# Kernel tuning notes

Measured on AMD Instinct MI355X. Metric: run time of the kernel, lower is better.

## Reference

```python
import jax, jax.numpy as jnp
import numpy as np

N = 50000      # nodes
E = 800000     # edges (avg degree 16)
IN = 128       # in_channels
OUT = 64       # out_channels
HID = 2 * OUT  # 128, hidden width of conv1
EPS = 1e-5     # BatchNorm eps


def _edge_norm(edge_index):
    # PyG ChebConv with sym normalization, lambda_max=2: L_hat = -D^{-1/2} A D^{-1/2}
    src, dst = edge_index[0], edge_index[1]
    deg = jax.ops.segment_sum(jnp.ones((E,), jnp.float32), src, num_segments=N)
    dinv = jnp.where(deg > 0, jax.lax.rsqrt(jnp.maximum(deg, 1.0)), 0.0)
    return -dinv[src] * dinv[dst]


def _cheb(x, src, dst, norm, W0, W1, b):
    # K=2 Chebyshev conv: Tx0 = x, Tx1 = L_hat x (sparse propagate)
    tx1 = jax.ops.segment_sum(x[src] * norm[:, None], dst, num_segments=N)
    return x @ W0 + tx1 @ W1 + b


def setup_inputs() -> dict:
    key = jax.random.key(0)
    ks = jax.random.split(key, 14)
    g = lambda k, shp, fan: jax.random.normal(k, shp, jnp.float32) / np.sqrt(fan)
    return {
        "x": jax.random.normal(ks[0], (N, IN), jnp.float32),
        "edge_index": jax.random.randint(ks[1], (2, E), 0, N, dtype=jnp.int32),
        "W1_0": g(ks[2], (IN, HID), IN),
        "W1_1": g(ks[3], (IN, HID), IN),
        "b1": jnp.zeros((HID,), jnp.float32),
        "gamma": jnp.ones((HID,), jnp.float32),
        "beta": jnp.zeros((HID,), jnp.float32),
        "Wmu_0": g(ks[4], (HID, OUT), HID),
        "Wmu_1": g(ks[5], (HID, OUT), HID),
        "b_mu": jnp.zeros((OUT,), jnp.float32),
        "Wls_0": g(ks[6], (HID, OUT), HID),
        "Wls_1": g(ks[7], (HID, OUT), HID),
        "b_ls": jnp.zeros((OUT,), jnp.float32),
    }


def reference(x, edge_index, W1_0, W1_1, b1, gamma, beta,
              Wmu_0, Wmu_1, b_mu, Wls_0, Wls_1, b_ls):
    src, dst = edge_index[0], edge_index[1]
    norm = _edge_norm(edge_index)
    h = _cheb(x, src, dst, norm, W1_0, W1_1, b1)         # [N, HID]
    # BatchNorm1d (training mode: batch statistics over nodes)
    mean = jnp.mean(h, axis=0)
    var = jnp.var(h, axis=0)
    h = (h - mean) * jax.lax.rsqrt(var + EPS) * gamma + beta
    h = jax.nn.relu(h)
    mu = _cheb(h, src, dst, norm, Wmu_0, Wmu_1, b_mu)    # [N, OUT]
    logstd = _cheb(h, src, dst, norm, Wls_0, Wls_1, b_ls)
    return (mu, logstd)
```

## Files before the change

kernel.cpp:

```cpp
#include <hip/hip_runtime.h>
#include <cstddef>
#include <cstdint>

static constexpr int IN_C  = 128;
static constexpr float BN_EPS = 1e-5f;
static constexpr int OUT_C = 64;

static constexpr int CS_C = 32;
static constexpr int CS_R = 8;
static constexpr int CS_RANGE = 6250;

using bf16x8 = __attribute__((ext_vector_type(8))) short;
using f32x4  = __attribute__((ext_vector_type(4))) float;

__device__ __forceinline__ ushort f2bf(float f) {
    uint u = __float_as_uint(f);
    u += 0x7fffu + ((u >> 16) & 1u);
    return (ushort)(u >> 16);
}
__device__ __forceinline__ uint pack2(float a, float b) {
    return (uint)f2bf(a) | ((uint)f2bf(b) << 16);
}
__device__ __forceinline__ float bf_lo(uint v) { return __uint_as_float(v << 16); }
__device__ __forceinline__ float bf_hi(uint v) { return __uint_as_float(v & 0xffff0000u); }

__device__ __forceinline__ int swz8(int row, int g) { return (g ^ ((row >> 1) & 3)) * 8; }

__global__ __launch_bounds__(1024) void hist_k(
    const int* __restrict__ src, const int* __restrict__ dst,
    int* __restrict__ hsrc_part, int* __restrict__ hdst_part,
    int N, int E, int chunk, int range) {
    __shared__ int hs_[CS_RANGE];
    __shared__ int hd_[CS_RANGE];
    int c = blockIdx.x & (CS_C - 1);
    int r = blockIdx.x / CS_C;
    int base = r * range;
    int hi = min(base + range, N);
    int rsz = hi - base;
    for (int j = threadIdx.x; j < rsz; j += 1024) { hs_[j] = 0; hd_[j] = 0; }
    __syncthreads();
    int e0 = c * chunk, e1 = min(e0 + chunk, E);
    for (int i = e0 + threadIdx.x; i < e1; i += 1024) {
        int s = src[i];
        if (s >= base && s < hi) atomicAdd(&hs_[s - base], 1);
        int t = dst[i];
        if (t >= base && t < hi) atomicAdd(&hd_[t - base], 1);
    }
    __syncthreads();
    for (int j = threadIdx.x; j < rsz; j += 1024) {
        hsrc_part[(size_t)c * N + base + j] = hs_[j];
        hdst_part[(size_t)c * N + base + j] = hd_[j];
    }
}

__global__ __launch_bounds__(256) void count_k(
    const int* __restrict__ hsrc_part, const int* __restrict__ hdst_part,
    float* __restrict__ dinv, int* __restrict__ cnt_dst,
    int* __restrict__ bsum, float* __restrict__ stats, int N) {
    __shared__ int sw[4];
    int tid = threadIdx.x;
    if (blockIdx.x == 0) stats[tid] = 0.f;
    int v = blockIdx.x * 256 + tid;
    int b = 0;
    if (v < N) {
        int a = 0;
        for (int c = 0; c < CS_C; ++c) {
            a += hsrc_part[(size_t)c * N + v];
            b += hdst_part[(size_t)c * N + v];
        }
        dinv[v] = (a > 0) ? rsqrtf((float)a) : 0.f;
        cnt_dst[v] = b;
    }
    int t = b;
    #pragma unroll
    for (int off = 1; off < 64; off <<= 1) t += __shfl_xor(t, off, 64);
    if ((tid & 63) == 0) sw[tid >> 6] = t;
    __syncthreads();
    if (tid == 0) bsum[blockIdx.x] = sw[0] + sw[1] + sw[2] + sw[3];
}

__global__ __launch_bounds__(256) void bscan_k(int* __restrict__ bsum, int nb) {
    __shared__ int sm[256];
    int tid = threadIdx.x;
    int v = (tid < nb) ? bsum[tid] : 0;
    sm[tid] = v;
    __syncthreads();
    #pragma unroll
    for (int off = 1; off < 256; off <<= 1) {
        int t = (tid >= off) ? sm[tid - off] : 0;
        __syncthreads();
        sm[tid] += t;
        __syncthreads();
    }
    if (tid < nb) bsum[tid] = sm[tid] - v;
}

__global__ __launch_bounds__(256) void phase3_k(
    const int* __restrict__ cnt, const int* __restrict__ bsum,
    int* __restrict__ row_ptr, int* __restrict__ hdst_part, int n) {
    __shared__ int swv[4];
    int tid = threadIdx.x;
    int lane = tid & 63, wave = tid >> 6;
    int v = blockIdx.x * 256 + tid;
    int c = (v < n) ? cnt[v] : 0;
    int s = c;
    #pragma unroll
    for (int off = 1; off < 64; off <<= 1) {
        int t = __shfl_up(s, off, 64);
        if (lane >= off) s += t;
    }
    if (lane == 63) swv[wave] = s;
    __syncthreads();
    int wexcl = 0;
    for (int w = 0; w < wave; ++w) wexcl += swv[w];
    int st = bsum[blockIdx.x] + wexcl + (s - c);
    if (v < n) row_ptr[v + 1] = st + c;
    if (v == 0) row_ptr[0] = 0;
    int r = st;
    for (int ch = 0; ch < CS_C; ++ch) {
        size_t idx = (size_t)ch * n + v;
        if (v < n) {
            int t = hdst_part[idx];
            hdst_part[idx] = r;
            r += t;
        }
    }
}

__global__ __launch_bounds__(1024) void scatter_k(
    const int* __restrict__ src, const int* __restrict__ dst,
    const int* __restrict__ off, int* __restrict__ col,
    int N, int E, int chunk, int range) {
    __shared__ int cur[CS_RANGE];
    int c = blockIdx.x & (CS_C - 1);
    int r = blockIdx.x / CS_C;
    int base = r * range;
    int hi = min(base + range, N);
    int rsz = hi - base;
    for (int j = threadIdx.x; j < rsz; j += 1024)
        cur[j] = off[(size_t)c * N + base + j];
    __syncthreads();
    int e0 = c * chunk, e1 = min(e0 + chunk, E);
    for (int i = e0 + threadIdx.x; i < e1; i += 1024) {
        int t = dst[i];
        if (t >= base && t < hi) {
            int pos = atomicAdd(&cur[t - base], 1);
            col[pos] = src[i];
        }
    }
}

__global__ void convert_prep_k(const float* __restrict__ in, const float* __restrict__ dinv,
                               ushort* __restrict__ xb, ushort* __restrict__ xsb, int n64,
                               int nb_conv,
                               const float* __restrict__ W1_0, const float* __restrict__ W1_1,
                               const float* __restrict__ b1,
                               const float* __restrict__ Wmu_0, const float* __restrict__ Wmu_1,
                               const float* __restrict__ b_mu,
                               const float* __restrict__ Wls_0, const float* __restrict__ Wls_1,
                               const float* __restrict__ b_ls,
                               ushort* __restrict__ Wt1, ushort* __restrict__ Wt2,
                               float* __restrict__ bias1, float* __restrict__ bias2) {
    int bid = blockIdx.x;
    if (bid < nb_conv) {
        int i = bid * 256 + threadIdx.x;
        if (i >= n64) return;
        int row = i >> 6;
        float d = dinv[row];
        float2 v = ((const float2*)in)[i];
        ((uint*)xb)[i] = pack2(v.x, v.y);
        ((uint*)xsb)[i] = pack2(v.x * d, v.y * d);
    } else {
        int idx = (bid - nb_conv) * 256 + threadIdx.x;
        int which = idx >> 15;
        int c = (idx >> 8) & 127;
        int k = idx & 255;
        if (which == 0) {
            float v = (k < 128) ? W1_0[k * 128 + c] : W1_1[(k - 128) * 128 + c];
            Wt1[c * 256 + k] = f2bf(v);
            if (k == 0) bias1[c] = b1[c];
        } else {
            float v;
            if (c < 64) v = (k < 128) ? Wmu_0[k * 64 + c] : Wmu_1[(k - 128) * 64 + c];
            else        v = (k < 128) ? Wls_0[k * 64 + (c - 64)] : Wls_1[(k - 128) * 64 + (c - 64)];
            Wt2[c * 256 + k] = f2bf(v);
            if (k == 0) bias2[c] = (c < 64) ? b_mu[c] : b_ls[c - 64];
        }
    }
}

#define ACC8(V)                                         \
    acc[0] += bf_lo((V).x); acc[1] += bf_hi((V).x);     \
    acc[2] += bf_lo((V).y); acc[3] += bf_hi((V).y);     \
    acc[4] += bf_lo((V).z); acc[5] += bf_hi((V).z);     \
    acc[6] += bf_lo((V).w); acc[7] += bf_hi((V).w);

__global__ __launch_bounds__(256) void propagate4_k(
    const uint4* __restrict__ xs, uint4* __restrict__ out,
    const int* __restrict__ row_ptr, const int* __restrict__ col,
    const float* __restrict__ dinv, int n) {
    int wid = (blockIdx.x * 256 + threadIdx.x) >> 6;
    if (wid >= n) return;
    int lane = threadIdx.x & 63;
    int g = lane >> 4, li = lane & 15;
    int s = row_ptr[wid], e = row_ptr[wid + 1];
    float acc[8];
    #pragma unroll
    for (int k = 0; k < 8; ++k) acc[k] = 0.f;
    int i = s + g;
    for (; i + 12 < e; i += 16) {
        int c0 = col[i];
        int c1 = col[i + 4];
        int c2 = col[i + 8];
        int c3 = col[i + 12];
        uint4 v0 = xs[(size_t)c0 * 16 + li];
        uint4 v1 = xs[(size_t)c1 * 16 + li];
        uint4 v2 = xs[(size_t)c2 * 16 + li];
        uint4 v3 = xs[(size_t)c3 * 16 + li];
        ACC8(v0); ACC8(v1); ACC8(v2); ACC8(v3);
    }
    for (; i < e; i += 4) {
        int c0 = col[i];
        uint4 v0 = xs[(size_t)c0 * 16 + li];
        ACC8(v0);
    }
    #pragma unroll
    for (int k = 0; k < 8; ++k) {
        acc[k] += __shfl_xor(acc[k], 16, 64);
        acc[k] += __shfl_xor(acc[k], 32, 64);
    }
    if (g == 0) {
        float sc = -dinv[wid];
        uint4 o;
        o.x = pack2(acc[0] * sc, acc[1] * sc);
        o.y = pack2(acc[2] * sc, acc[3] * sc);
        o.z = pack2(acc[4] * sc, acc[5] * sc);
        o.w = pack2(acc[6] * sc, acc[7] * sc);
        out[(size_t)wid * 16 + li] = o;
    }
}

template <int MODE>
__global__ __launch_bounds__(256) void gemm_mfma_k(
    const ushort* __restrict__ A0, const ushort* __restrict__ A1,
    const ushort* __restrict__ Wt, const float* __restrict__ bias,
    ushort* __restrict__ Cb, float* __restrict__ Cmu, float* __restrict__ Cls,
    float* __restrict__ stats, int n) {
    __shared__ ushort sA[64][32];
    __shared__ ushort sW[128][32];
    __shared__ float smS[4][128];
    __shared__ float smQ[4][128];

    int tid = threadIdx.x;
    int block_row = blockIdx.x * 64;
    int wave = tid >> 6, lane = tid & 63;
    int col_base = lane & 15;
    int quad = lane >> 4;
    int m_local = wave * 16 + col_base;

    f32x4 acc[8];
    #pragma unroll
    for (int t = 0; t < 8; ++t) acc[t] = (f32x4){0.f, 0.f, 0.f, 0.f};

    for (int k0 = 0; k0 < 256; k0 += 32) {
        {
            int row = tid >> 2, g = tid & 3;
            int grow = block_row + row;
            int kc = k0 + g * 8;
            uint4 v = make_uint4(0, 0, 0, 0);
            if (grow < n) {
                const ushort* srcp = (kc < 128) ? (A0 + (size_t)grow * 128 + kc)
                                                : (A1 + (size_t)grow * 128 + (kc - 128));
                v = *(const uint4*)srcp;
            }
            *(uint4*)&sA[row][swz8(row, g)] = v;
        }
        #pragma unroll
        for (int i = tid; i < 512; i += 256) {
            int c = i >> 2, g = i & 3;
            *(uint4*)&sW[c][swz8(c, g)] = *(const uint4*)(Wt + (size_t)c * 256 + k0 + g * 8);
        }
        __syncthreads();
        bf16x8 af = *(const bf16x8*)&sA[m_local][swz8(m_local, quad)];
        #pragma unroll
        for (int t = 0; t < 8; ++t) {
            int wr = t * 16 + col_base;
            bf16x8 bfr = *(const bf16x8*)&sW[wr][swz8(wr, quad)];
            acc[t] = __builtin_amdgcn_mfma_f32_16x16x32_bf16(af, bfr, acc[t], 0, 0, 0);
        }
        __syncthreads();
    }

    int row_l = wave * 16 + quad * 4;
    #pragma unroll
    for (int t = 0; t < 8; ++t) {
        int col = t * 16 + col_base;
        float b = bias[col];
        float s = 0.f, q = 0.f;
        #pragma unroll
        for (int r = 0; r < 4; ++r) {
            int grow = block_row + row_l + r;
            if (grow < n) {
                float v = acc[t][r] + b;
                if (MODE == 0) {
                    Cb[(size_t)grow * 128 + col] = f2bf(v);
                    s += v; q += v * v;
                } else {
                    if (col < 64) Cmu[(size_t)grow * 64 + col] = v;
                    else          Cls[(size_t)grow * 64 + (col - 64)] = v;
                }
            }
        }
        if (MODE == 0) {
            s += __shfl_xor(s, 16, 64); s += __shfl_xor(s, 32, 64);
            q += __shfl_xor(q, 16, 64); q += __shfl_xor(q, 32, 64);
            if (quad == 0) { smS[wave][col] = s; smQ[wave][col] = q; }
        }
    }
    if (MODE == 0) {
        __syncthreads();
        if (tid < 128) {
            float s = smS[0][tid] + smS[1][tid] + smS[2][tid] + smS[3][tid];
            float q = smQ[0][tid] + smQ[1][tid] + smQ[2][tid] + smQ[3][tid];
            atomicAdd(&stats[tid], s);
            atomicAdd(&stats[128 + tid], q);
        }
    }
}

__global__ __launch_bounds__(256) void bn_apply_k(
    ushort* __restrict__ hb, ushort* __restrict__ hsb,
    const float* __restrict__ stats, const float* __restrict__ gamma,
    const float* __restrict__ beta, const float* __restrict__ dinv,
    float inv_n, int n64) {
    __shared__ float sp[256];
    int tid = threadIdx.x;
    if (tid < 128) {
        float mean = stats[tid] * inv_n;
        float var = stats[128 + tid] * inv_n - mean * mean;
        float sc = gamma[tid] * rsqrtf(var + BN_EPS);
        sp[tid] = sc;
        sp[128 + tid] = beta[tid] - mean * sc;
    }
    __syncthreads();
    int i = blockIdx.x * 256 + tid;
    if (i >= n64) return;
    int c2 = (i & 63) * 2;
    int row = i >> 6;
    uint v = ((uint*)hb)[i];
    float f0 = fmaxf(bf_lo(v) * sp[c2]     + sp[128 + c2],     0.f);
    float f1 = fmaxf(bf_hi(v) * sp[c2 + 1] + sp[128 + c2 + 1], 0.f);
    ((uint*)hb)[i] = pack2(f0, f1);
    float d = dinv[row];
    ((uint*)hsb)[i] = pack2(f0 * d, f1 * d);
}

extern "C" void kernel_launch(void* const* d_in, const int* in_sizes, int n_in,
                              void* d_out, int out_size, void* d_ws, size_t ws_size,
                              hipStream_t stream) {
    const float* x = (const float*)d_in[0];
    const int* edge_index = (const int*)d_in[1];
    const float* W1_0 = (const float*)d_in[2];
    const float* W1_1 = (const float*)d_in[3];
    const float* b1 = (const float*)d_in[4];
    const float* gamma = (const float*)d_in[5];
    const float* beta = (const float*)d_in[6];
    const float* Wmu_0 = (const float*)d_in[7];
    const float* Wmu_1 = (const float*)d_in[8];
    const float* b_mu = (const float*)d_in[9];
    const float* Wls_0 = (const float*)d_in[10];
    const float* Wls_1 = (const float*)d_in[11];
    const float* b_ls = (const float*)d_in[12];

    const int N = in_sizes[0] / IN_C;
    const int E = in_sizes[1] / 2;
    const int* src = edge_index;
    const int* dst = edge_index + E;

    char* w = (char*)d_ws;
    auto alloc = [&](size_t bytes) {
        char* p = w;
        w += (bytes + 15) & ~(size_t)15;
        return p;
    };
    float* stats = (float*)alloc(256 * 4);
    int* row_ptr = (int*)alloc((size_t)(N + 1) * 4);
    int* bsum    = (int*)alloc(256 * 4);
    float* dinv  = (float*)alloc((size_t)N * 4);
    int* cnt_dst = (int*)alloc((size_t)N * 4);
    int* col     = (int*)alloc((size_t)E * 4);
    int* hsrc_part = (int*)alloc((size_t)CS_C * N * 4);
    int* hdst_part = (int*)alloc((size_t)CS_C * N * 4);
    ushort* x_bf  = (ushort*)alloc((size_t)N * 128 * 2);
    ushort* xs_bf = (ushort*)alloc((size_t)N * 128 * 2);
    ushort* xp_bf = (ushort*)alloc((size_t)N * 128 * 2);
    ushort* h_bf  = (ushort*)alloc((size_t)N * 128 * 2);
    ushort* Wt1   = (ushort*)alloc(128 * 256 * 2);
    ushort* Wt2   = (ushort*)alloc(128 * 256 * 2);
    float* bias1  = (float*)alloc(128 * 4);
    float* bias2  = (float*)alloc(128 * 4);

    ushort* hs_bf = xs_bf;
    ushort* hp_bf = xp_bf;

    float* out_mu = (float*)d_out;
    float* out_ls = out_mu + (size_t)N * OUT_C;

    int chunk = (E + CS_C - 1) / CS_C;
    int range = (N + CS_R - 1) / CS_R;
    int NBLK = (N + 255) / 256;
    int nb_conv = (N * 64 + 255) / 256;

    hist_k<<<CS_R * CS_C, 1024, 0, stream>>>(src, dst, hsrc_part, hdst_part, N, E, chunk, range);
    count_k<<<NBLK, 256, 0, stream>>>(hsrc_part, hdst_part, dinv, cnt_dst, bsum, stats, N);
    bscan_k<<<1, 256, 0, stream>>>(bsum, NBLK);
    phase3_k<<<NBLK, 256, 0, stream>>>(cnt_dst, bsum, row_ptr, hdst_part, N);
    scatter_k<<<CS_R * CS_C, 1024, 0, stream>>>(src, dst, hdst_part, col, N, E, chunk, range);

    convert_prep_k<<<nb_conv + 256, 256, 0, stream>>>(
        x, dinv, x_bf, xs_bf, N * 64, nb_conv,
        W1_0, W1_1, b1, Wmu_0, Wmu_1, b_mu, Wls_0, Wls_1, b_ls,
        Wt1, Wt2, bias1, bias2);

    int pb = (N + 3) / 4;
    propagate4_k<<<pb, 256, 0, stream>>>((const uint4*)xs_bf, (uint4*)xp_bf,
                                         row_ptr, col, dinv, N);

    int gb = (N + 63) / 64;
    gemm_mfma_k<0><<<gb, 256, 0, stream>>>(x_bf, xp_bf, Wt1, bias1, h_bf,
                                           nullptr, nullptr, stats, N);

    bn_apply_k<<<(N * 64 + 255) / 256, 256, 0, stream>>>(h_bf, hs_bf, stats, gamma, beta,
                                                         dinv, 1.f / (float)N, N * 64);

    propagate4_k<<<pb, 256, 0, stream>>>((const uint4*)hs_bf, (uint4*)hp_bf,
                                         row_ptr, col, dinv, N);

    gemm_mfma_k<1><<<gb, 256, 0, stream>>>(h_bf, hp_bf, Wt2, bias2, nullptr,
                                           out_mu, out_ls, stats, N);
}
```

Measured before the change: 293.4 us.

## Fuse histogram with input conversion, drop prescaled copies, fold block scan into phase3

The x and weight bf16 conversion moves into the histogram kernel as extra blocks, so it no longer waits for dinv and saves one launch. The dinv-prescaled copies of x and h are no longer written. Propagation instead loads dinv[col] per edge and multiplies it in, trading one extra gather per edge for less write traffic. The separate block-scan kernel is removed: each phase3 block sums the preceding block totals itself. Per-chunk histograms are stored as ushort to cut their memory traffic, which assumes no chunk holds more than 65535 edges for one node.

```diff
diff --git a/kernel.cpp b/kernel.cpp
--- a/kernel.cpp
+++ b/kernel.cpp
@@ -26,35 +26,69 @@
 
 __device__ __forceinline__ int swz8(int row, int g) { return (g ^ ((row >> 1) & 3)) * 8; }
 
-__global__ __launch_bounds__(1024) void hist_k(
+__global__ __launch_bounds__(1024) void hist_conv_k(
     const int* __restrict__ src, const int* __restrict__ dst,
-    int* __restrict__ hsrc_part, int* __restrict__ hdst_part,
-    int N, int E, int chunk, int range) {
+    ushort* __restrict__ hsrc_part, ushort* __restrict__ hdst_part,
+    int N, int E, int chunk, int range, int nb_hist, int nb_x,
+    const float* __restrict__ x, ushort* __restrict__ xb,
+    const float* __restrict__ W1_0, const float* __restrict__ W1_1,
+    const float* __restrict__ b1,
+    const float* __restrict__ Wmu_0, const float* __restrict__ Wmu_1,
+    const float* __restrict__ b_mu,
+    const float* __restrict__ Wls_0, const float* __restrict__ Wls_1,
+    const float* __restrict__ b_ls,
+    ushort* __restrict__ Wt1, ushort* __restrict__ Wt2,
+    float* __restrict__ bias1, float* __restrict__ bias2) {
     __shared__ int hs_[CS_RANGE];
     __shared__ int hd_[CS_RANGE];
-    int c = blockIdx.x & (CS_C - 1);
-    int r = blockIdx.x / CS_C;
-    int base = r * range;
-    int hi = min(base + range, N);
-    int rsz = hi - base;
-    for (int j = threadIdx.x; j < rsz; j += 1024) { hs_[j] = 0; hd_[j] = 0; }
-    __syncthreads();
-    int e0 = c * chunk, e1 = min(e0 + chunk, E);
-    for (int i = e0 + threadIdx.x; i < e1; i += 1024) {
-        int s = src[i];
-        if (s >= base && s < hi) atomicAdd(&hs_[s - base], 1);
-        int t = dst[i];
-        if (t >= base && t < hi) atomicAdd(&hd_[t - base], 1);
-    }
-    __syncthreads();
-    for (int j = threadIdx.x; j < rsz; j += 1024) {
-        hsrc_part[(size_t)c * N + base + j] = hs_[j];
-        hdst_part[(size_t)c * N + base + j] = hd_[j];
+    int bid = blockIdx.x;
+    if (bid < nb_hist) {
+        int c = bid & (CS_C - 1);
+        int r = bid / CS_C;
+        int base = r * range;
+        int hi = min(base + range, N);
+        int rsz = hi - base;
+        for (int j = threadIdx.x; j < rsz; j += 1024) { hs_[j] = 0; hd_[j] = 0; }
+        __syncthreads();
+        int e0 = c * chunk, e1 = min(e0 + chunk, E);
+        for (int i = e0 + threadIdx.x; i < e1; i += 1024) {
+            int s = src[i];
+            if (s >= base && s < hi) atomicAdd(&hs_[s - base], 1);
+            int t = dst[i];
+            if (t >= base && t < hi) atomicAdd(&hd_[t - base], 1);
+        }
+        __syncthreads();
+        for (int j = threadIdx.x; j < rsz; j += 1024) {
+            hsrc_part[(size_t)c * N + base + j] = (ushort)hs_[j];
+            hdst_part[(size_t)c * N + base + j] = (ushort)hd_[j];
+        }
+    } else if (bid < nb_hist + nb_x) {
+        int i = (bid - nb_hist) * 1024 + threadIdx.x;
+        if (i < N * 64) {
+            float2 v = ((const float2*)x)[i];
+            ((uint*)xb)[i] = pack2(v.x, v.y);
+        }
+    } else {
+        int idx = (bid - nb_hist - nb_x) * 1024 + threadIdx.x;
+        int which = idx >> 15;
+        int c = (idx >> 8) & 127;
+        int k = idx & 255;
+        if (which == 0) {
+            float v = (k < 128) ? W1_0[k * 128 + c] : W1_1[(k - 128) * 128 + c];
+            Wt1[c * 256 + k] = f2bf(v);
+            if (k == 0) bias1[c] = b1[c];
+        } else {
+            float v;
+            if (c < 64) v = (k < 128) ? Wmu_0[k * 64 + c] : Wmu_1[(k - 128) * 64 + c];
+            else        v = (k < 128) ? Wls_0[k * 64 + (c - 64)] : Wls_1[(k - 128) * 64 + (c - 64)];
+            Wt2[c * 256 + k] = f2bf(v);
+            if (k == 0) bias2[c] = (c < 64) ? b_mu[c] : b_ls[c - 64];
+        }
     }
 }
 
 __global__ __launch_bounds__(256) void count_k(
-    const int* __restrict__ hsrc_part, const int* __restrict__ hdst_part,
+    const ushort* __restrict__ hsrc_part, const ushort* __restrict__ hdst_part,
     float* __restrict__ dinv, int* __restrict__ cnt_dst,
     int* __restrict__ bsum, float* __restrict__ stats, int N) {
     __shared__ int sw[4];
@@ -79,50 +113,41 @@
     if (tid == 0) bsum[blockIdx.x] = sw[0] + sw[1] + sw[2] + sw[3];
 }
 
-__global__ __launch_bounds__(256) void bscan_k(int* __restrict__ bsum, int nb) {
-    __shared__ int sm[256];
-    int tid = threadIdx.x;
-    int v = (tid < nb) ? bsum[tid] : 0;
-    sm[tid] = v;
-    __syncthreads();
-    #pragma unroll
-    for (int off = 1; off < 256; off <<= 1) {
-        int t = (tid >= off) ? sm[tid - off] : 0;
-        __syncthreads();
-        sm[tid] += t;
-        __syncthreads();
-    }
-    if (tid < nb) bsum[tid] = sm[tid] - v;
-}
-
 __global__ __launch_bounds__(256) void phase3_k(
     const int* __restrict__ cnt, const int* __restrict__ bsum,
-    int* __restrict__ row_ptr, int* __restrict__ hdst_part, int n) {
+    int* __restrict__ row_ptr, const ushort* __restrict__ hdst_part,
+    int* __restrict__ offs, int n, int nb) {
+    __shared__ int sbp[4];
     __shared__ int swv[4];
     int tid = threadIdx.x;
     int lane = tid & 63, wave = tid >> 6;
+    int bv = (tid < nb && tid < (int)blockIdx.x) ? bsum[tid] : 0;
+    int t = bv;
+    #pragma unroll
+    for (int off = 1; off < 64; off <<= 1) t += __shfl_xor(t, off, 64);
+    if (lane == 0) sbp[wave] = t;
     int v = blockIdx.x * 256 + tid;
     int c = (v < n) ? cnt[v] : 0;
     int s = c;
     #pragma unroll
     for (int off = 1; off < 64; off <<= 1) {
-        int t = __shfl_up(s, off, 64);
-        if (lane >= off) s += t;
+        int u = __shfl_up(s, off, 64);
+        if (lane >= off) s += u;
     }
     if (lane == 63) swv[wave] = s;
     __syncthreads();
+    int bpre = sbp[0] + sbp[1] + sbp[2] + sbp[3];
     int wexcl = 0;
     for (int w = 0; w < wave; ++w) wexcl += swv[w];
-    int st = bsum[blockIdx.x] + wexcl + (s - c);
+    int st = bpre + wexcl + (s - c);
     if (v < n) row_ptr[v + 1] = st + c;
     if (v == 0) row_ptr[0] = 0;
     int r = st;
     for (int ch = 0; ch < CS_C; ++ch) {
         size_t idx = (size_t)ch * n + v;
         if (v < n) {
-            int t = hdst_part[idx];
-            hdst_part[idx] = r;
-            r += t;
+            offs[idx] = r;
+            r += hdst_part[idx];
         }
     }
 }
@@ -150,50 +175,11 @@
     }
 }
 
-__global__ void convert_prep_k(const float* __restrict__ in, const float* __restrict__ dinv,
-                               ushort* __restrict__ xb, ushort* __restrict__ xsb, int n64,
-                               int nb_conv,
-                               const float* __restrict__ W1_0, const float* __restrict__ W1_1,
-                               const float* __restrict__ b1,
-                               const float* __restrict__ Wmu_0, const float* __restrict__ Wmu_1,
-                               const float* __restrict__ b_mu,
-                               const float* __restrict__ Wls_0, const float* __restrict__ Wls_1,
-                               const float* __restrict__ b_ls,
-                               ushort* __restrict__ Wt1, ushort* __restrict__ Wt2,
-                               float* __restrict__ bias1, float* __restrict__ bias2) {
-    int bid = blockIdx.x;
-    if (bid < nb_conv) {
-        int i = bid * 256 + threadIdx.x;
-        if (i >= n64) return;
-        int row = i >> 6;
-        float d = dinv[row];
-        float2 v = ((const float2*)in)[i];
-        ((uint*)xb)[i] = pack2(v.x, v.y);
-        ((uint*)xsb)[i] = pack2(v.x * d, v.y * d);
-    } else {
-        int idx = (bid - nb_conv) * 256 + threadIdx.x;
-        int which = idx >> 15;
-        int c = (idx >> 8) & 127;
-        int k = idx & 255;
-        if (which == 0) {
-            float v = (k < 128) ? W1_0[k * 128 + c] : W1_1[(k - 128) * 128 + c];
-            Wt1[c * 256 + k] = f2bf(v);
-            if (k == 0) bias1[c] = b1[c];
-        } else {
-            float v;
-            if (c < 64) v = (k < 128) ? Wmu_0[k * 64 + c] : Wmu_1[(k - 128) * 64 + c];
-            else        v = (k < 128) ? Wls_0[k * 64 + (c - 64)] : Wls_1[(k - 128) * 64 + (c - 64)];
-            Wt2[c * 256 + k] = f2bf(v);
-            if (k == 0) bias2[c] = (c < 64) ? b_mu[c] : b_ls[c - 64];
-        }
-    }
-}
-
-#define ACC8(V)                                         \
-    acc[0] += bf_lo((V).x); acc[1] += bf_hi((V).x);     \
-    acc[2] += bf_lo((V).y); acc[3] += bf_hi((V).y);     \
-    acc[4] += bf_lo((V).z); acc[5] += bf_hi((V).z);     \
-    acc[6] += bf_lo((V).w); acc[7] += bf_hi((V).w);
+#define FMA8(V, D)                                                 \
+    acc[0] += bf_lo((V).x) * (D); acc[1] += bf_hi((V).x) * (D);    \
+    acc[2] += bf_lo((V).y) * (D); acc[3] += bf_hi((V).y) * (D);    \
+    acc[4] += bf_lo((V).z) * (D); acc[5] += bf_hi((V).z) * (D);    \
+    acc[6] += bf_lo((V).w) * (D); acc[7] += bf_hi((V).w) * (D);
 
 __global__ __launch_bounds__(256) void propagate4_k(
     const uint4* __restrict__ xs, uint4* __restrict__ out,
@@ -213,16 +199,18 @@
         int c1 = col[i + 4];
         int c2 = col[i + 8];
         int c3 = col[i + 12];
+        float d0 = dinv[c0], d1 = dinv[c1], d2 = dinv[c2], d3 = dinv[c3];
         uint4 v0 = xs[(size_t)c0 * 16 + li];
         uint4 v1 = xs[(size_t)c1 * 16 + li];
         uint4 v2 = xs[(size_t)c2 * 16 + li];
         uint4 v3 = xs[(size_t)c3 * 16 + li];
-        ACC8(v0); ACC8(v1); ACC8(v2); ACC8(v3);
+        FMA8(v0, d0); FMA8(v1, d1); FMA8(v2, d2); FMA8(v3, d3);
     }
     for (; i < e; i += 4) {
         int c0 = col[i];
+        float d0 = dinv[c0];
         uint4 v0 = xs[(size_t)c0 * 16 + li];
-        ACC8(v0);
+        FMA8(v0, d0);
     }
     #pragma unroll
     for (int k = 0; k < 8; ++k) {
@@ -329,9 +317,8 @@
 }
 
 __global__ __launch_bounds__(256) void bn_apply_k(
-    ushort* __restrict__ hb, ushort* __restrict__ hsb,
-    const float* __restrict__ stats, const float* __restrict__ gamma,
-    const float* __restrict__ beta, const float* __restrict__ dinv,
+    ushort* __restrict__ hb, const float* __restrict__ stats,
+    const float* __restrict__ gamma, const float* __restrict__ beta,
     float inv_n, int n64) {
     __shared__ float sp[256];
     int tid = threadIdx.x;
@@ -346,13 +333,10 @@
     int i = blockIdx.x * 256 + tid;
     if (i >= n64) return;
     int c2 = (i & 63) * 2;
-    int row = i >> 6;
     uint v = ((uint*)hb)[i];
     float f0 = fmaxf(bf_lo(v) * sp[c2]     + sp[128 + c2],     0.f);
     float f1 = fmaxf(bf_hi(v) * sp[c2 + 1] + sp[128 + c2 + 1], 0.f);
     ((uint*)hb)[i] = pack2(f0, f1);
-    float d = dinv[row];
-    ((uint*)hsb)[i] = pack2(f0 * d, f1 * d);
 }
 
 extern "C" void kernel_launch(void* const* d_in, const int* in_sizes, int n_in,
@@ -389,10 +373,10 @@
     float* dinv  = (float*)alloc((size_t)N * 4);
     int* cnt_dst = (int*)alloc((size_t)N * 4);
     int* col     = (int*)alloc((size_t)E * 4);
-    int* hsrc_part = (int*)alloc((size_t)CS_C * N * 4);
-    int* hdst_part = (int*)alloc((size_t)CS_C * N * 4);
+    ushort* hsrc_part = (ushort*)alloc((size_t)CS_C * N * 2);
+    ushort* hdst_part = (ushort*)alloc((size_t)CS_C * N * 2);
+    int* offs    = (int*)alloc((size_t)CS_C * N * 4);
     ushort* x_bf  = (ushort*)alloc((size_t)N * 128 * 2);
-    ushort* xs_bf = (ushort*)alloc((size_t)N * 128 * 2);
     ushort* xp_bf = (ushort*)alloc((size_t)N * 128 * 2);
     ushort* h_bf  = (ushort*)alloc((size_t)N * 128 * 2);
     ushort* Wt1   = (ushort*)alloc(128 * 256 * 2);
@@ -400,42 +384,38 @@
     float* bias1  = (float*)alloc(128 * 4);
     float* bias2  = (float*)alloc(128 * 4);
 
-    ushort* hs_bf = xs_bf;
-    ushort* hp_bf = xp_bf;
-
     float* out_mu = (float*)d_out;
     float* out_ls = out_mu + (size_t)N * OUT_C;
 
     int chunk = (E + CS_C - 1) / CS_C;
     int range = (N + CS_R - 1) / CS_R;
     int NBLK = (N + 255) / 256;
-    int nb_conv = (N * 64 + 255) / 256;
-
-    hist_k<<<CS_R * CS_C, 1024, 0, stream>>>(src, dst, hsrc_part, hdst_part, N, E, chunk, range);
+    int nb_hist = CS_R * CS_C;
+    int nb_x = (N * 64 + 1023) / 1024;
+    int nb_w = 64;
+
+    hist_conv_k<<<nb_hist + nb_x + nb_w, 1024, 0, stream>>>(
+        src, dst, hsrc_part, hdst_part, N, E, chunk, range, nb_hist, nb_x,
+        x, x_bf, W1_0, W1_1, b1, Wmu_0, Wmu_1, b_mu, Wls_0, Wls_1, b_ls,
+        Wt1, Wt2, bias1, bias2);
     count_k<<<NBLK, 256, 0, stream>>>(hsrc_part, hdst_part, dinv, cnt_dst, bsum, stats, N);
-    bscan_k<<<1, 256, 0, stream>>>(bsum, NBLK);
-    phase3_k<<<NBLK, 256, 0, stream>>>(cnt_dst, bsum, row_ptr, hdst_part, N);
-    scatter_k<<<CS_R * CS_C, 1024, 0, stream>>>(src, dst, hdst_part, col, N, E, chunk, range);
-
-    convert_prep_k<<<nb_conv + 256, 256, 0, stream>>>(
-        x, dinv, x_bf, xs_bf, N * 64, nb_conv,
-        W1_0, W1_1, b1, Wmu_0, Wmu_1, b_mu, Wls_0, Wls_1, b_ls,
-        Wt1, Wt2, bias1, bias2);
+    phase3_k<<<NBLK, 256, 0, stream>>>(cnt_dst, bsum, row_ptr, hdst_part, offs, N, NBLK);
+    scatter_k<<<nb_hist, 1024, 0, stream>>>(src, dst, offs, col, N, E, chunk, range);
 
     int pb = (N + 3) / 4;
-    propagate4_k<<<pb, 256, 0, stream>>>((const uint4*)xs_bf, (uint4*)xp_bf,
+    propagate4_k<<<pb, 256, 0, stream>>>((const uint4*)x_bf, (uint4*)xp_bf,
                                          row_ptr, col, dinv, N);
 
     int gb = (N + 63) / 64;
     gemm_mfma_k<0><<<gb, 256, 0, stream>>>(x_bf, xp_bf, Wt1, bias1, h_bf,
                                            nullptr, nullptr, stats, N);
 
-    bn_apply_k<<<(N * 64 + 255) / 256, 256, 0, stream>>>(h_bf, hs_bf, stats, gamma, beta,
-                                                         dinv, 1.f / (float)N, N * 64);
-
-    propagate4_k<<<pb, 256, 0, stream>>>((const uint4*)hs_bf, (uint4*)hp_bf,
+    bn_apply_k<<<(N * 64 + 255) / 256, 256, 0, stream>>>(h_bf, stats, gamma, beta,
+                                                         1.f / (float)N, N * 64);
+
+    propagate4_k<<<pb, 256, 0, stream>>>((const uint4*)h_bf, (uint4*)xp_bf,
                                          row_ptr, col, dinv, N);
 
-    gemm_mfma_k<1><<<gb, 256, 0, stream>>>(h_bf, hp_bf, Wt2, bias2, nullptr,
+    gemm_mfma_k<1><<<gb, 256, 0, stream>>>(h_bf, xp_bf, Wt2, bias2, nullptr,
                                            out_mu, out_ls, stats, N);
 }
```

New measurement: 279.5 us. -4.7%, faster.
